# Kernel optimization log

Measured on AMD Instinct MI355X. Metric: run time of the kernel, lower is better.

The kernel has to match this reference:

```python
import jax, jax.numpy as jnp
import numpy as np
import math

B, T, E, H = 4, 2048, 1024, 16
D = E // H

def setup_inputs() -> dict:
    key = jax.random.key(0)
    k1, k2, k3 = jax.random.split(key, 3)
    x = jax.random.normal(k1, (B, T, E), dtype=jnp.float32)
    # GPT-2 Conv1D: out = x @ W + b, W shape [in, out]
    W_attn = jax.random.normal(k2, (E, 3 * E), dtype=jnp.float32) * 0.02
    b_attn = jnp.zeros((3 * E,), dtype=jnp.float32)
    W_proj = jax.random.normal(k3, (E, E), dtype=jnp.float32) * 0.02
    b_proj = jnp.zeros((E,), dtype=jnp.float32)
    # causal mask, broadcastable [1,1,T,T]; masked where mask == 0
    mask = jnp.tril(jnp.ones((T, T), dtype=jnp.int32))[None, None]
    return {"x": x, "mask": mask, "W_attn": W_attn, "b_attn": b_attn,
            "W_proj": W_proj, "b_proj": b_proj}

def reference(x, mask, W_attn, b_attn, W_proj, b_proj):
    Bx, Tx, Ex = x.shape
    qkv = x @ W_attn + b_attn                      # [B,T,3E]
    q, k, v = jnp.split(qkv, 3, axis=-1)
    q = q.reshape(Bx, Tx, H, D)
    k = k.reshape(Bx, Tx, H, D)
    v = v.reshape(Bx, Tx, H, D)
    att = jnp.einsum('bqhd,bkhd->bhqk', q, k) / math.sqrt(D)
    att = jnp.where(mask == 0, jnp.float32(-1e20), att)
    att = jax.nn.softmax(att, axis=-1)
    y = jnp.einsum('bhqk,bkhd->bqhd', att, v).reshape(Bx, Tx, Ex)
    y = y @ W_proj + b_proj
    return y
```

## Files before the change

kernel.cpp:

```cpp
#include <hip/hip_runtime.h>
#include <hip/hip_bf16.h>

#define BB 4
#define TT 2048
#define EE 1024
#define HH 16
#define DD 64
#define PART_SZ (BB*HH*TT*DD)

typedef __bf16 bf16x8_t __attribute__((ext_vector_type(8)));
typedef float floatx4_t __attribute__((ext_vector_type(4)));

__device__ __forceinline__ unsigned short f2bf(float f) {
    union { float f; unsigned int i; } v; v.f = f;
    unsigned int x = v.i;
    return (unsigned short)((x + 0x7FFFu + ((x >> 16) & 1u)) >> 16);
}
__device__ __forceinline__ unsigned int cvt_pk_bf16(float lo, float hi) {
    unsigned int r;
    asm("v_cvt_pk_bf16_f32 %0, %1, %2" : "=v"(r) : "v"(lo), "v"(hi));
    return r;
}

typedef __attribute__((address_space(1))) const unsigned int gu32_t;
typedef __attribute__((address_space(3))) unsigned int lu32_t;
__device__ __forceinline__ void gl_lds16(const unsigned short* g, unsigned short* l) {
    __builtin_amdgcn_global_load_lds((gu32_t*)g, (lu32_t*)l, 16, 0, 0);
}

__global__ __launch_bounds__(256)
void prepass_k(const float* __restrict__ x, unsigned short* __restrict__ xb,
               const float* __restrict__ Wa, unsigned short* __restrict__ WaT,
               const float* __restrict__ Wp, unsigned short* __restrict__ WpT)
{
    __shared__ unsigned short L[64 * 72];
    const int id  = blockIdx.x;
    const int tid = threadIdx.x;

    if (id < 4096) {
        const size_t i = ((size_t)id * 256 + tid) * 8;
        float4 a = *(const float4*)(x + i);
        float4 b = *(const float4*)(x + i + 4);
        uint4 p;
        p.x = cvt_pk_bf16(a.x, a.y); p.y = cvt_pk_bf16(a.z, a.w);
        p.z = cvt_pk_bf16(b.x, b.y); p.w = cvt_pk_bf16(b.z, b.w);
        *(uint4*)(xb + i) = p;
        return;
    }

    const float* W;
    unsigned short* WT;
    int N, tn, tk;
    if (id < 4096 + 768) {
        const int t = id - 4096;
        W = Wa; WT = WaT; N = 3072;
        tn = (t % 48) * 64; tk = (t / 48) * 64;
    } else {
        const int t = id - 4864;
        W = Wp; WT = WpT; N = 1024;
        tn = (t % 16) * 64; tk = (t / 16) * 64;
    }
    {
        const int k  = tid >> 2;
        const int n0 = (tid & 3) * 16;
        const float* src = W + (size_t)(tk + k) * N + tn + n0;
        float4 f0 = *(const float4*)(src);
        float4 f1 = *(const float4*)(src + 4);
        float4 f2 = *(const float4*)(src + 8);
        float4 f3 = *(const float4*)(src + 12);
        uint4 p0, p1;
        p0.x = cvt_pk_bf16(f0.x, f0.y); p0.y = cvt_pk_bf16(f0.z, f0.w);
        p0.z = cvt_pk_bf16(f1.x, f1.y); p0.w = cvt_pk_bf16(f1.z, f1.w);
        p1.x = cvt_pk_bf16(f2.x, f2.y); p1.y = cvt_pk_bf16(f2.z, f2.w);
        p1.z = cvt_pk_bf16(f3.x, f3.y); p1.w = cvt_pk_bf16(f3.z, f3.w);
        *(uint4*)(&L[k * 72 + n0])     = p0;
        *(uint4*)(&L[k * 72 + n0 + 8]) = p1;
    }
    __syncthreads();
    {
        const int n  = tid >> 2;
        const int k0 = (tid & 3) * 16;
        unsigned short u[16];
        #pragma unroll
        for (int e = 0; e < 16; e++) u[e] = L[(k0 + e) * 72 + n];
        unsigned short* dst = WT + (size_t)(tn + n) * 1024 + tk + k0;
        *(uint4*)(dst)     = *(uint4*)&u[0];
        *(uint4*)(dst + 8) = *(uint4*)&u[8];
    }
}

template<int MODE>
__global__ __launch_bounds__(256, 2)
void gemm_k(const unsigned short* __restrict__ Ag,
            const unsigned short* __restrict__ Wt,
            const float* __restrict__ biasg,
            unsigned short* __restrict__ Qo,
            unsigned short* __restrict__ Ko,
            unsigned short* __restrict__ Vo,
            float* __restrict__ Fo)
{
    constexpr int N = (MODE == 0) ? 3072 : 1024;
    __shared__ unsigned short Al[2][128 * 32];
    __shared__ unsigned short Bl[2][128 * 32];
    constexpr size_t EPSZ = (MODE == 0) ? (4 * 16 * 72 * 2) : (4 * 16 * 68 * 4);
    __shared__ __align__(16) char EpRaw[EPSZ];
    const int tid  = threadIdx.x;
    int bn, bm;
    if (MODE == 0) {
        const int id = blockIdx.x;
        const int s  = id & 7;
        const int t  = id >> 3;
        const int P  = (t / 12) * 8 + s;
        bm = (P >> 1) * 128;
        bn = ((P & 1) * 12 + (t % 12)) * 128;
    } else {
        const int id = blockIdx.x;
        const int s  = id & 7;
        const int t  = id >> 3;
        bm = ((t & 7) * 8 + s) * 128;
        bn = (t >> 3) * 128;
    }
    const int lane = tid & 63;
    const int wv   = tid >> 6;
    const int wm   = (wv & 1) * 64;
    const int wn   = (wv >> 1) * 64;
    const int l16  = lane & 15;
    const int quad = lane >> 4;
    const int lrow = lane >> 2;
    const int lk   = (lane & 3) * 8;

    const bool flip = (MODE == 1) || (bn < 2 * EE);

    floatx4_t acc[4][4];
    #pragma unroll
    for (int i = 0; i < 4; i++)
        #pragma unroll
        for (int j = 0; j < 4; j++)
            acc[i][j] = (floatx4_t){0.f, 0.f, 0.f, 0.f};

    for (int k0 = 0; k0 < 1024; k0 += 64) {
        __syncthreads();
        #pragma unroll
        for (int t = 0; t < 2; t++) {
            const int rb = wv * 32 + t * 16;
            const unsigned short* as = Ag + (size_t)(bm + rb + lrow) * 1024 + k0 + lk;
            const unsigned short* bs = Wt + (size_t)(bn + rb + lrow) * 1024 + k0 + lk;
            gl_lds16(as,      &Al[0][rb * 32]);
            gl_lds16(bs,      &Bl[0][rb * 32]);
            gl_lds16(as + 32, &Al[1][rb * 32]);
            gl_lds16(bs + 32, &Bl[1][rb * 32]);
        }
        __syncthreads();

        #pragma unroll
        for (int h = 0; h < 2; h++) {
            bf16x8_t af[4], bfr[4];
            #pragma unroll
            for (int i = 0; i < 4; i++)
                af[i]  = *(const bf16x8_t*)(&Al[h][(wm + i * 16 + l16) * 32 + quad * 8]);
            #pragma unroll
            for (int j = 0; j < 4; j++)
                bfr[j] = *(const bf16x8_t*)(&Bl[h][(wn + j * 16 + l16) * 32 + quad * 8]);
            if (flip) {
                #pragma unroll
                for (int u = 0; u < 4; u++)
                    #pragma unroll
                    for (int v = 0; v < 4; v++)
                        acc[u][v] = __builtin_amdgcn_mfma_f32_16x16x32_bf16(bfr[u], af[v], acc[u][v], 0, 0, 0);
            } else {
                #pragma unroll
                for (int u = 0; u < 4; u++)
                    #pragma unroll
                    for (int v = 0; v < 4; v++)
                        acc[u][v] = __builtin_amdgcn_mfma_f32_16x16x32_bf16(af[u], bfr[v], acc[u][v], 0, 0, 0);
            }
        }
    }

    const int rdrow = lane >> 2;
    const int rdseg = (lane & 3) * 16;

    if (MODE == 1) {
        float* Epf = (float*)EpRaw + wv * 16 * 68;
        floatx4_t bv[4];
        #pragma unroll
        for (int u = 0; u < 4; u++)
            bv[u] = *(const floatx4_t*)(biasg + bn + wn + u * 16 + quad * 4);
        #pragma unroll
        for (int v = 0; v < 4; v++) {
            #pragma unroll
            for (int u = 0; u < 4; u++) {
                floatx4_t val;
                #pragma unroll
                for (int rr = 0; rr < 4; rr++) val[rr] = acc[u][v][rr] + bv[u][rr];
                *(floatx4_t*)(&Epf[l16 * 68 + u * 16 + quad * 4]) = val;
            }
            __builtin_amdgcn_s_waitcnt(0);
            const int m = bm + wm + v * 16 + rdrow;
            float* dst = Fo + (size_t)m * N + bn + wn + rdseg;
            const float* srcl = &Epf[rdrow * 68 + rdseg];
            #pragma unroll
            for (int c = 0; c < 4; c++)
                *(floatx4_t*)(dst + c * 4) = *(const floatx4_t*)(srcl + c * 4);
        }
    } else if (flip) {
        unsigned short* Ep = (unsigned short*)EpRaw + wv * 16 * 72;
        floatx4_t bv[4];
        #pragma unroll
        for (int u = 0; u < 4; u++)
            bv[u] = *(const floatx4_t*)(biasg + bn + wn + u * 16 + quad * 4);
        const int p  = bn >> 10;
        const int h  = ((bn + wn) & 1023) >> 6;
        const int d0 = rdseg & 63;
        unsigned short* outb = (p == 0) ? Qo : Ko;
        const float sc = (p == 0) ? 0.18033688f : 1.0f;
        #pragma unroll
        for (int v = 0; v < 4; v++) {
            #pragma unroll
            for (int u = 0; u < 4; u++) {
                uint2 pk;
                pk.x = cvt_pk_bf16((acc[u][v][0] + bv[u][0]) * sc, (acc[u][v][1] + bv[u][1]) * sc);
                pk.y = cvt_pk_bf16((acc[u][v][2] + bv[u][2]) * sc, (acc[u][v][3] + bv[u][3]) * sc);
                *(uint2*)(&Ep[l16 * 72 + u * 16 + quad * 4]) = pk;
            }
            __builtin_amdgcn_s_waitcnt(0);
            const int t  = bm + wm + v * 16 + rdrow;
            const int b_ = t >> 11, t_ = t & 2047;
            unsigned short* dst = outb + ((size_t)(b_ * HH + h) * TT + t_) * DD + d0;
            const unsigned short* srcl = &Ep[rdrow * 72 + rdseg];
            *(uint4*)(dst)     = *(const uint4*)(srcl);
            *(uint4*)(dst + 8) = *(const uint4*)(srcl + 8);
        }
    } else {
        unsigned short* Ep = (unsigned short*)EpRaw + wv * 16 * 72;
        #pragma unroll
        for (int v = 0; v < 4; v++) {
            const float bias_v = biasg[bn + wn + v * 16 + l16];
            #pragma unroll
            for (int u = 0; u < 4; u++) {
                uint2 pk;
                pk.x = cvt_pk_bf16(acc[u][v][0] + bias_v, acc[u][v][1] + bias_v);
                pk.y = cvt_pk_bf16(acc[u][v][2] + bias_v, acc[u][v][3] + bias_v);
                *(uint2*)(&Ep[l16 * 72 + u * 16 + quad * 4]) = pk;
            }
            __builtin_amdgcn_s_waitcnt(0);
            const int n  = bn + wn + v * 16 + rdrow;
            const int h  = (n & 1023) >> 6, d = n & 63;
            const int t0 = bm + wm + rdseg;
            const int b_ = t0 >> 11, t_ = t0 & 2047;
            unsigned short* dst = Vo + ((size_t)(b_ * HH + h) * DD + d) * TT + t_;
            const unsigned short* srcl = &Ep[rdrow * 72 + rdseg];
            *(uint4*)(dst)     = *(const uint4*)(srcl);
            *(uint4*)(dst + 8) = *(const uint4*)(srcl + 8);
        }
    }
}

__global__ __launch_bounds__(256, 4)
void attn_k(const unsigned short* __restrict__ Qg,
            const unsigned short* __restrict__ Kg,
            const unsigned short* __restrict__ Vg,
            unsigned short* __restrict__ Og)
{
    __shared__ unsigned short Kt[64 * 72];
    __shared__ unsigned short Vt[64 * 72];
    __shared__ unsigned short Pw[4][16 * 72];
    const int tid  = threadIdx.x;
    const int w    = tid >> 6;
    const int lane = tid & 63;
    const int l16  = lane & 15;
    const int quad = lane >> 4;
    const int id = blockIdx.x;
    const int t_ = id >> 3;
    const int J  = (t_ & 15) ^ (((t_ >> 5) & 3) << 2);
    const int bh = (id & 7) + 8 * (t_ >> 4);
    const int qb0 = J * 64;
    const int qb1 = (31 - J) * 64;
    const int qw0 = qb0 + w * 16;
    const int qw1 = qb1 + w * 16;
    const size_t base = (size_t)bh * TT * DD;

    bf16x8_t qf0[2], qf1[2];
    #pragma unroll
    for (int ks = 0; ks < 2; ks++) {
        qf0[ks] = *(const bf16x8_t*)(Qg + base + (size_t)(qw0 + l16) * DD + ks * 32 + quad * 8);
        qf1[ks] = *(const bf16x8_t*)(Qg + base + (size_t)(qw1 + l16) * DD + ks * 32 + quad * 8);
    }

    union { unsigned int u[4]; bf16x8_t v; } ones;
    #pragma unroll
    for (int i = 0; i < 4; i++) ones.u[i] = 0x3F803F80u;

    floatx4_t oacc0[4], oacc1[4];
    #pragma unroll
    for (int n = 0; n < 4; n++) {
        oacc0[n] = (floatx4_t){0.f, 0.f, 0.f, 0.f};
        oacc1[n] = (floatx4_t){0.f, 0.f, 0.f, 0.f};
    }
    floatx4_t dacc0 = (floatx4_t){0.f, 0.f, 0.f, 0.f};
    floatx4_t dacc1 = (floatx4_t){0.f, 0.f, 0.f, 0.f};

    const int kend = qb1 + 64;
    const int srow = tid >> 2;
    const int sc0  = (tid & 3) * 16;
    const int kqb  = quad * 4;
    const int qq0  = qw0 + l16;
    const int qq1  = qw1 + l16;

    auto COMP = [&](int kb, int qw, int qq, const bf16x8_t* qf,
                    floatx4_t* oacc, floatx4_t& dacc) {
        if (kb < qw + 16) {
            floatx4_t sacc[4];
            #pragma unroll
            for (int n = 0; n < 4; n++) sacc[n] = (floatx4_t){0.f, 0.f, 0.f, 0.f};
            __builtin_amdgcn_s_setprio(1);
            #pragma unroll
            for (int n = 0; n < 4; n++) {
                #pragma unroll
                for (int ks = 0; ks < 2; ks++) {
                    bf16x8_t kf = *(const bf16x8_t*)(&Kt[(n * 16 + l16) * 72 + ks * 32 + quad * 8]);
                    sacc[n] = __builtin_amdgcn_mfma_f32_16x16x32_bf16(kf, qf[ks], sacc[n], 0, 0, 0);
                }
            }
            __builtin_amdgcn_s_setprio(0);
            if ((kb + 63) > qw) {
                #pragma unroll
                for (int n = 0; n < 4; n++) {
                    const int keyb = kb + n * 16 + kqb;
                    #pragma unroll
                    for (int rr = 0; rr < 4; rr++)
                        if (keyb + rr > qq) sacc[n][rr] = -1e30f;
                }
            }
            #pragma unroll
            for (int n = 0; n < 4; n++) {
                const float p0 = __builtin_exp2f(sacc[n][0]);
                const float p1 = __builtin_exp2f(sacc[n][1]);
                const float p2 = __builtin_exp2f(sacc[n][2]);
                const float p3 = __builtin_exp2f(sacc[n][3]);
                uint2 pk;
                pk.x = cvt_pk_bf16(p0, p1);
                pk.y = cvt_pk_bf16(p2, p3);
                *(uint2*)(&Pw[w][l16 * 72 + n * 16 + kqb]) = pk;
            }
            bf16x8_t pf[2];
            #pragma unroll
            for (int ks = 0; ks < 2; ks++)
                pf[ks] = *(const bf16x8_t*)(&Pw[w][l16 * 72 + ks * 32 + quad * 8]);
            __builtin_amdgcn_s_setprio(1);
            #pragma unroll
            for (int ks = 0; ks < 2; ks++)
                dacc = __builtin_amdgcn_mfma_f32_16x16x32_bf16(pf[ks], ones.v, dacc, 0, 0, 0);
            #pragma unroll
            for (int n = 0; n < 4; n++) {
                #pragma unroll
                for (int ks = 0; ks < 2; ks++) {
                    bf16x8_t vf = *(const bf16x8_t*)(&Vt[(n * 16 + l16) * 72 + ks * 32 + quad * 8]);
                    oacc[n] = __builtin_amdgcn_mfma_f32_16x16x32_bf16(pf[ks], vf, oacc[n], 0, 0, 0);
                }
            }
            __builtin_amdgcn_s_setprio(0);
        }
    };

    const unsigned short* kg0 = Kg + base + (size_t)srow * DD + sc0;
    const unsigned short* vg0 = Vg + base + (size_t)srow * TT + sc0;

    uint4 rk0 = *(const uint4*)(kg0);
    uint4 rk1 = *(const uint4*)(kg0 + 8);
    uint4 rv0 = *(const uint4*)(vg0);
    uint4 rv1 = *(const uint4*)(vg0 + 8);

    for (int kb = 0; kb < kend; kb += 64) {
        __syncthreads();
        *(uint4*)(&Kt[srow * 72 + sc0])     = rk0;
        *(uint4*)(&Kt[srow * 72 + sc0 + 8]) = rk1;
        *(uint4*)(&Vt[srow * 72 + sc0])     = rv0;
        *(uint4*)(&Vt[srow * 72 + sc0 + 8]) = rv1;
        if (kb + 64 < kend) {
            const unsigned short* kg = kg0 + (size_t)(kb + 64) * DD;
            const unsigned short* vg = vg0 + kb + 64;
            rk0 = *(const uint4*)(kg);
            rk1 = *(const uint4*)(kg + 8);
            rv0 = *(const uint4*)(vg);
            rv1 = *(const uint4*)(vg + 8);
        }
        __syncthreads();
        COMP(kb, qw0, qq0, qf0, oacc0, dacc0);
        COMP(kb, qw1, qq1, qf1, oacc1, dacc1);
    }

    const int b_ = bh >> 4, h_ = bh & 15;
    auto EPI = [&](int qw, const floatx4_t& dacc, const floatx4_t* oacc) {
        #pragma unroll
        for (int rr = 0; rr < 4; rr++) {
            const float inv = 1.f / dacc[rr];
            const int q = qw + quad * 4 + rr;
            unsigned short* op = Og + (((size_t)b_ * TT + q) * HH + h_) * DD;
            #pragma unroll
            for (int n = 0; n < 4; n++)
                op[n * 16 + l16] = f2bf(oacc[n][rr] * inv);
        }
    };
    EPI(qw0, dacc0, oacc0);
    EPI(qw1, dacc1, oacc1);
}

extern "C" void kernel_launch(void* const* d_in, const int* in_sizes, int n_in,
                              void* d_out, int out_size, void* d_ws, size_t ws_size,
                              hipStream_t stream) {
    const float* x      = (const float*)d_in[0];
    const float* W_attn = (const float*)d_in[2];
    const float* b_attn = (const float*)d_in[3];
    const float* W_proj = (const float*)d_in[4];
    const float* b_proj = (const float*)d_in[5];
    float* out = (float*)d_out;

    unsigned short* Qs  = (unsigned short*)d_out;
    unsigned short* Ks  = Qs + (size_t)PART_SZ;
    unsigned short* VTs = (unsigned short*)d_ws;
    unsigned short* Ao  = VTs + (size_t)PART_SZ;
    unsigned short* Xb  = Ao + (size_t)PART_SZ;
    unsigned short* WaT = Xb + (size_t)PART_SZ;
    unsigned short* WpT = WaT + (size_t)3072 * 1024;

    prepass_k<<<5120, 256, 0, stream>>>(x, Xb, W_attn, WaT, W_proj, WpT);

    gemm_k<0><<<1536, 256, 0, stream>>>(Xb, WaT, b_attn, Qs, Ks, VTs, nullptr);

    attn_k<<<1024, 256, 0, stream>>>(Qs, Ks, VTs, Ao);

    gemm_k<1><<<512, 256, 0, stream>>>(Ao, WpT, b_proj, nullptr, nullptr, nullptr, out);
}
```

Before: 265.0 us.

## Double-buffer GEMM LDS staging with manual vmcnt waits and lighter barriers

```diff
diff --git a/kernel.cpp b/kernel.cpp
--- a/kernel.cpp
+++ b/kernel.cpp
@@ -26,6 +26,12 @@
 typedef __attribute__((address_space(3))) unsigned int lu32_t;
 __device__ __forceinline__ void gl_lds16(const unsigned short* g, unsigned short* l) {
     __builtin_amdgcn_global_load_lds((gu32_t*)g, (lu32_t*)l, 16, 0, 0);
+}
+
+__device__ __forceinline__ void block_barrier() {
+    asm volatile("" ::: "memory");
+    __builtin_amdgcn_s_barrier();
+    asm volatile("" ::: "memory");
 }
 
 __global__ __launch_bounds__(256)
@@ -138,44 +144,59 @@
         for (int j = 0; j < 4; j++)
             acc[i][j] = (floatx4_t){0.f, 0.f, 0.f, 0.f};
 
+#define STAGE(BUF, K0) do {                                                        \
+        _Pragma("unroll")                                                          \
+        for (int t = 0; t < 2; t++) {                                              \
+            const int rb = wv * 32 + t * 16;                                       \
+            gl_lds16(Ag + (size_t)(bm + rb + lrow) * 1024 + (K0) + lk,             \
+                     &Al[BUF][rb * 32]);                                           \
+            gl_lds16(Wt + (size_t)(bn + rb + lrow) * 1024 + (K0) + lk,             \
+                     &Bl[BUF][rb * 32]);                                           \
+        }                                                                          \
+    } while (0)
+
+#define COMP32(H) do {                                                             \
+        bf16x8_t af[4], bfr[4];                                                    \
+        _Pragma("unroll")                                                          \
+        for (int i = 0; i < 4; i++)                                                \
+            af[i]  = *(const bf16x8_t*)(&Al[H][(wm + i * 16 + l16) * 32 + quad * 8]); \
+        _Pragma("unroll")                                                          \
+        for (int j = 0; j < 4; j++)                                                \
+            bfr[j] = *(const bf16x8_t*)(&Bl[H][(wn + j * 16 + l16) * 32 + quad * 8]); \
+        if (flip) {                                                                \
+            _Pragma("unroll")                                                      \
+            for (int u = 0; u < 4; u++)                                            \
+                _Pragma("unroll")                                                  \
+                for (int v = 0; v < 4; v++)                                        \
+                    acc[u][v] = __builtin_amdgcn_mfma_f32_16x16x32_bf16(bfr[u], af[v], acc[u][v], 0, 0, 0); \
+        } else {                                                                   \
+            _Pragma("unroll")                                                      \
+            for (int u = 0; u < 4; u++)                                            \
+                _Pragma("unroll")                                                  \
+                for (int v = 0; v < 4; v++)                                        \
+                    acc[u][v] = __builtin_amdgcn_mfma_f32_16x16x32_bf16(af[u], bfr[v], acc[u][v], 0, 0, 0); \
+        }                                                                          \
+    } while (0)
+
+    STAGE(0, 0);
     for (int k0 = 0; k0 < 1024; k0 += 64) {
-        __syncthreads();
-        #pragma unroll
-        for (int t = 0; t < 2; t++) {
-            const int rb = wv * 32 + t * 16;
-            const unsigned short* as = Ag + (size_t)(bm + rb + lrow) * 1024 + k0 + lk;
-            const unsigned short* bs = Wt + (size_t)(bn + rb + lrow) * 1024 + k0 + lk;
-            gl_lds16(as,      &Al[0][rb * 32]);
-            gl_lds16(bs,      &Bl[0][rb * 32]);
-            gl_lds16(as + 32, &Al[1][rb * 32]);
-            gl_lds16(bs + 32, &Bl[1][rb * 32]);
-        }
-        __syncthreads();
-
-        #pragma unroll
-        for (int h = 0; h < 2; h++) {
-            bf16x8_t af[4], bfr[4];
-            #pragma unroll
-            for (int i = 0; i < 4; i++)
-                af[i]  = *(const bf16x8_t*)(&Al[h][(wm + i * 16 + l16) * 32 + quad * 8]);
-            #pragma unroll
-            for (int j = 0; j < 4; j++)
-                bfr[j] = *(const bf16x8_t*)(&Bl[h][(wn + j * 16 + l16) * 32 + quad * 8]);
-            if (flip) {
-                #pragma unroll
-                for (int u = 0; u < 4; u++)
-                    #pragma unroll
-                    for (int v = 0; v < 4; v++)
-                        acc[u][v] = __builtin_amdgcn_mfma_f32_16x16x32_bf16(bfr[u], af[v], acc[u][v], 0, 0, 0);
-            } else {
-                #pragma unroll
-                for (int u = 0; u < 4; u++)
-                    #pragma unroll
-                    for (int v = 0; v < 4; v++)
-                        acc[u][v] = __builtin_amdgcn_mfma_f32_16x16x32_bf16(af[u], bfr[v], acc[u][v], 0, 0, 0);
-            }
-        }
-    }
+        STAGE(1, k0 + 32);
+        asm volatile("s_waitcnt vmcnt(4)" ::: "memory");
+        block_barrier();
+        COMP32(0);
+        block_barrier();
+        if (k0 + 64 < 1024) {
+            STAGE(0, k0 + 64);
+            asm volatile("s_waitcnt vmcnt(4)" ::: "memory");
+        } else {
+            asm volatile("s_waitcnt vmcnt(0)" ::: "memory");
+        }
+        block_barrier();
+        COMP32(1);
+        block_barrier();
+    }
+#undef STAGE
+#undef COMP32
 
     const int rdrow = lane >> 2;
     const int rdseg = (lane & 3) * 16;
@@ -372,7 +393,7 @@
     uint4 rv1 = *(const uint4*)(vg0 + 8);
 
     for (int kb = 0; kb < kend; kb += 64) {
-        __syncthreads();
+        block_barrier();
         *(uint4*)(&Kt[srow * 72 + sc0])     = rk0;
         *(uint4*)(&Kt[srow * 72 + sc0 + 8]) = rk1;
         *(uint4*)(&Vt[srow * 72 + sc0])     = rv0;
@@ -385,7 +406,8 @@
             rv0 = *(const uint4*)(vg);
             rv1 = *(const uint4*)(vg + 8);
         }
-        __syncthreads();
+        asm volatile("s_waitcnt lgkmcnt(0)" ::: "memory");
+        block_barrier();
         COMP(kb, qw0, qq0, qf0, oacc0, dacc0);
         COMP(kb, qw1, qq1, qf1, oacc1, dacc1);
     }
```

Result: slower. 278.4 us (+5.1%).

## Load V fragments directly from global and double-buffer K in LDS

Applied to the files above, without the earlier changes.

```diff
diff --git a/kernel.cpp b/kernel.cpp
--- a/kernel.cpp
+++ b/kernel.cpp
@@ -262,8 +262,7 @@
             const unsigned short* __restrict__ Vg,
             unsigned short* __restrict__ Og)
 {
-    __shared__ unsigned short Kt[64 * 72];
-    __shared__ unsigned short Vt[64 * 72];
+    __shared__ unsigned short Kt[2][64 * 72];
     __shared__ unsigned short Pw[4][16 * 72];
     const int tid  = threadIdx.x;
     const int w    = tid >> 6;
@@ -308,6 +307,7 @@
     const int qq1  = qw1 + l16;
 
     auto COMP = [&](int kb, int qw, int qq, const bf16x8_t* qf,
+                    const bf16x8_t (*vf)[2], const unsigned short* KtC,
                     floatx4_t* oacc, floatx4_t& dacc) {
         if (kb < qw + 16) {
             floatx4_t sacc[4];
@@ -318,7 +318,7 @@
             for (int n = 0; n < 4; n++) {
                 #pragma unroll
                 for (int ks = 0; ks < 2; ks++) {
-                    bf16x8_t kf = *(const bf16x8_t*)(&Kt[(n * 16 + l16) * 72 + ks * 32 + quad * 8]);
+                    bf16x8_t kf = *(const bf16x8_t*)(&KtC[(n * 16 + l16) * 72 + ks * 32 + quad * 8]);
                     sacc[n] = __builtin_amdgcn_mfma_f32_16x16x32_bf16(kf, qf[ks], sacc[n], 0, 0, 0);
                 }
             }
@@ -354,40 +354,39 @@
             #pragma unroll
             for (int n = 0; n < 4; n++) {
                 #pragma unroll
-                for (int ks = 0; ks < 2; ks++) {
-                    bf16x8_t vf = *(const bf16x8_t*)(&Vt[(n * 16 + l16) * 72 + ks * 32 + quad * 8]);
-                    oacc[n] = __builtin_amdgcn_mfma_f32_16x16x32_bf16(pf[ks], vf, oacc[n], 0, 0, 0);
-                }
+                for (int ks = 0; ks < 2; ks++)
+                    oacc[n] = __builtin_amdgcn_mfma_f32_16x16x32_bf16(pf[ks], vf[n][ks], oacc[n], 0, 0, 0);
             }
             __builtin_amdgcn_s_setprio(0);
         }
     };
 
     const unsigned short* kg0 = Kg + base + (size_t)srow * DD + sc0;
-    const unsigned short* vg0 = Vg + base + (size_t)srow * TT + sc0;
+    const unsigned short* vb  = Vg + base + (size_t)l16 * TT + quad * 8;
 
     uint4 rk0 = *(const uint4*)(kg0);
     uint4 rk1 = *(const uint4*)(kg0 + 8);
-    uint4 rv0 = *(const uint4*)(vg0);
-    uint4 rv1 = *(const uint4*)(vg0 + 8);
-
+
+    int buf = 0;
     for (int kb = 0; kb < kend; kb += 64) {
-        __syncthreads();
-        *(uint4*)(&Kt[srow * 72 + sc0])     = rk0;
-        *(uint4*)(&Kt[srow * 72 + sc0 + 8]) = rk1;
-        *(uint4*)(&Vt[srow * 72 + sc0])     = rv0;
-        *(uint4*)(&Vt[srow * 72 + sc0 + 8]) = rv1;
+        unsigned short* KtC = Kt[buf];
+        *(uint4*)(&KtC[srow * 72 + sc0])     = rk0;
+        *(uint4*)(&KtC[srow * 72 + sc0 + 8]) = rk1;
         if (kb + 64 < kend) {
             const unsigned short* kg = kg0 + (size_t)(kb + 64) * DD;
-            const unsigned short* vg = vg0 + kb + 64;
             rk0 = *(const uint4*)(kg);
             rk1 = *(const uint4*)(kg + 8);
-            rv0 = *(const uint4*)(vg);
-            rv1 = *(const uint4*)(vg + 8);
         }
         __syncthreads();
-        COMP(kb, qw0, qq0, qf0, oacc0, dacc0);
-        COMP(kb, qw1, qq1, qf1, oacc1, dacc1);
+        bf16x8_t vf[4][2];
+        #pragma unroll
+        for (int n = 0; n < 4; n++)
+            #pragma unroll
+            for (int ks = 0; ks < 2; ks++)
+                vf[n][ks] = *(const bf16x8_t*)(vb + (size_t)(n * 16) * TT + kb + ks * 32);
+        COMP(kb, qw0, qq0, qf0, vf, KtC, oacc0, dacc0);
+        COMP(kb, qw1, qq1, qf1, vf, KtC, oacc1, dacc1);
+        buf ^= 1;
     }
 
     const int b_ = bh >> 4, h_ = bh & 15;
```

Result: slower. 353.8 us (+33.5%).
